# Optimization experiments

Hardware: AMD Instinct MI355X
Metric: run time of the kernel (lower is better)

Reference implementation:

```python
import jax, jax.numpy as jnp
import numpy as np

N_NODES = 10000
N_EDGES = 320000
D_IN = 256
D_OUT = 256
MAX_NORM = 0.95

def setup_inputs() -> dict:
    key = jax.random.key(0)
    ks = jax.random.split(key, 7)
    x = jax.random.normal(ks[0], (N_NODES, D_IN), dtype=jnp.float32)
    edge_index = jax.random.randint(ks[1], (2, N_EDGES), 0, N_NODES, dtype=jnp.int64)
    # xavier-ish scales
    W = jax.random.normal(ks[2], (D_OUT, D_IN), dtype=jnp.float32) * (1.0 / np.sqrt(D_IN))
    b = jax.random.normal(ks[3], (D_OUT,), dtype=jnp.float32) * 0.02
    mag_w = jax.random.normal(ks[4], (1, D_IN), dtype=jnp.float32) * 0.02
    mag_b = jax.random.normal(ks[5], (1,), dtype=jnp.float32) * 0.02
    attn_w = jax.random.normal(ks[6], (1, 2 * D_OUT), dtype=jnp.float32) * (1.0 / np.sqrt(2 * D_OUT))
    return {"x": x, "edge_index": edge_index, "W": W, "b": b,
            "mag_w": mag_w, "mag_b": mag_b, "attn_w": attn_w}

def _expmap0(u):
    # Poincare ball exp map at origin, curvature c = 1.0
    un = jnp.linalg.norm(u, axis=-1, keepdims=True)
    un_c = jnp.maximum(un, 1e-15)
    return jnp.tanh(un_c) * u / un_c

def reference(x, edge_index, W, b, mag_w, mag_b, attn_w):
    N = x.shape[0]
    F_out = W.shape[0]
    # linear transform + directional/magnitude decomposition
    h_raw = x @ W.T + b                                              # (N, F)
    h_dir = h_raw / jnp.maximum(jnp.linalg.norm(h_raw, axis=-1, keepdims=True), 1e-12)
    h_mag = jax.nn.sigmoid(x @ mag_w.T + mag_b) * 1.5                # (N, 1)
    h = h_dir * h_mag                                                # (N, F)
    src, tgt = edge_index[0], edge_index[1]
    h_src = h[src]                                                   # (E, F)
    h_tgt = h[tgt]                                                   # (E, F)
    # attn(cat([h_src, h_tgt])) == h_src @ a_s + h_tgt @ a_t (avoids concat)
    a_s, a_t = attn_w[0, :F_out], attn_w[0, F_out:]
    scores = h_src @ a_s + h_tgt @ a_t                               # (E,)
    # scatter softmax over edges grouped by target node
    mx = jnp.maximum(jax.ops.segment_max(scores, tgt, num_segments=N), -1e9)
    ex = jnp.exp(scores - mx[tgt])
    se = jax.ops.segment_sum(ex, tgt, num_segments=N)
    attn_weights = ex / (se[tgt] + 1e-10)                            # (E,)
    # weighted message aggregation
    agg = jax.ops.segment_sum(h_src * attn_weights[:, None], tgt, num_segments=N)
    h_combined = h + agg
    h_poincare = _expmap0(h_combined)
    norms = jnp.linalg.norm(h_poincare, axis=1, keepdims=True)
    return jnp.where(norms > MAX_NORM, h_poincare * (MAX_NORM / (norms + 1e-8)), h_poincare)
```

## Files before the change

### kernel.cpp

```cpp
#include <hip/hip_runtime.h>
#include <math.h>

#define N_NODES 10000
#define N_EDGES 320000
#define D 256
#define CAP 128
#define BM 32
#define LDK 40

typedef __attribute__((ext_vector_type(8))) short short8;
typedef __attribute__((ext_vector_type(4))) float f32x4;

__device__ __forceinline__ ushort f2bf(float f) {
    union { float f; unsigned u; } v; v.f = f;
    unsigned r = v.u + 0x7FFFu + ((v.u >> 16) & 1u);
    return (ushort)(r >> 16);
}
__device__ __forceinline__ float bf2f(ushort u) {
    union { unsigned u; float f; } v; v.u = (unsigned)u << 16;
    return v.f;
}

__global__ __launch_bounds__(256) void k_prep(const float* __restrict__ W,
                                              ushort* __restrict__ Wb) {
    const int i = (blockIdx.x * 256 + threadIdx.x) * 4;
    const float4 v = *(const float4*)&W[i];
    ushort4 o;
    o.x = f2bf(v.x); o.y = f2bf(v.y); o.z = f2bf(v.z); o.w = f2bf(v.w);
    *(ushort4*)&Wb[i] = o;
}

__global__ __launch_bounds__(256) void k_gemm_fused(const float* __restrict__ x,
                                                    const ushort* __restrict__ Wb,
                                                    const float* __restrict__ b,
                                                    const float* __restrict__ mag_w,
                                                    const float* __restrict__ mag_b,
                                                    const float* __restrict__ attn_w,
                                                    ushort* __restrict__ hb,
                                                    float* __restrict__ s_s,
                                                    float* __restrict__ s_t,
                                                    unsigned* __restrict__ deg) {
    __shared__ ushort ldsA[BM * LDK];
    __shared__ ushort ldsB[256 * LDK];
    __shared__ float red_ssq[4][BM], red_ra[4][BM], red_rt[4][BM];
    __shared__ float smrow[BM], scl[BM];

    const int t = threadIdx.x;
    const int w = t >> 6, l = t & 63;
    const int bm = blockIdx.x * BM;
    const int sra = t >> 3, ka = (t & 7) * 4;
    const int am = bm + sra;
    const int srb = t >> 2, kb = (t & 3) * 8;

    const int fl = l & 15;
    const int fh = (l >> 4) * 8;

    f32x4 acc[2][4];
#pragma unroll
    for (int r = 0; r < 2; ++r)
#pragma unroll
        for (int c = 0; c < 4; ++c) acc[r][c] = (f32x4)(0.f);

    float sm_part = 0.f;

    for (int k0 = 0; k0 < D; k0 += 32) {
        float4 xa = make_float4(0.f, 0.f, 0.f, 0.f);
        if (am < N_NODES) xa = *(const float4*)&x[(size_t)am * D + k0 + ka];
        const float4 mwv = *(const float4*)&mag_w[k0 + ka];
        sm_part += xa.x * mwv.x + xa.y * mwv.y + xa.z * mwv.z + xa.w * mwv.w;
        short8 bv[4];
#pragma unroll
        for (int p = 0; p < 4; ++p)
            bv[p] = *(const short8*)&Wb[(size_t)(p * 64 + srb) * D + k0 + kb];
        __syncthreads();
        ushort4 av;
        av.x = f2bf(xa.x); av.y = f2bf(xa.y); av.z = f2bf(xa.z); av.w = f2bf(xa.w);
        *(ushort4*)&ldsA[sra * LDK + ka] = av;
#pragma unroll
        for (int p = 0; p < 4; ++p)
            *(short8*)&ldsB[(p * 64 + srb) * LDK + kb] = bv[p];
        __syncthreads();
        short8 af[2], bfr[4];
#pragma unroll
        for (int r = 0; r < 2; ++r)
            af[r] = *(short8*)&ldsA[(r * 16 + fl) * LDK + fh];
#pragma unroll
        for (int c = 0; c < 4; ++c)
            bfr[c] = *(short8*)&ldsB[(w * 64 + c * 16 + fl) * LDK + fh];
#pragma unroll
        for (int r = 0; r < 2; ++r)
#pragma unroll
            for (int c = 0; c < 4; ++c)
                acc[r][c] = __builtin_amdgcn_mfma_f32_16x16x32_bf16(af[r], bfr[c], acc[r][c], 0, 0, 0);
    }

#pragma unroll
    for (int o = 1; o < 8; o <<= 1) sm_part += __shfl_xor(sm_part, o);
    if ((t & 7) == 0) smrow[sra] = sm_part;

    float bn[4], asn[4], atn[4];
#pragma unroll
    for (int c = 0; c < 4; ++c) {
        const int n = w * 64 + c * 16 + fl;
        bn[c]  = b[n];
        asn[c] = attn_w[n];
        atn[c] = attn_w[D + n];
    }
    const int rq = (l >> 4) * 4;

#pragma unroll
    for (int r = 0; r < 2; ++r) {
#pragma unroll
        for (int reg = 0; reg < 4; ++reg) {
            float vssq = 0.f, vra = 0.f, vrt = 0.f;
#pragma unroll
            for (int c = 0; c < 4; ++c) {
                const float v = acc[r][c][reg] + bn[c];
                vssq += v * v;
                vra  += v * asn[c];
                vrt  += v * atn[c];
            }
#pragma unroll
            for (int o = 1; o < 16; o <<= 1) {
                vssq += __shfl_xor(vssq, o);
                vra  += __shfl_xor(vra, o);
                vrt  += __shfl_xor(vrt, o);
            }
            if (fl == 0) {
                const int m = r * 16 + rq + reg;
                red_ssq[w][m] = vssq;
                red_ra[w][m]  = vra;
                red_rt[w][m]  = vrt;
            }
        }
    }
    __syncthreads();

    if (t < BM) {
        const int gm = bm + t;
        const float ssq = red_ssq[0][t] + red_ssq[1][t] + red_ssq[2][t] + red_ssq[3][t];
        const float ra  = red_ra[0][t]  + red_ra[1][t]  + red_ra[2][t]  + red_ra[3][t];
        const float rt  = red_rt[0][t]  + red_rt[1][t]  + red_rt[2][t]  + red_rt[3][t];
        const float norm = sqrtf(ssq);
        const float mag  = 1.5f / (1.f + expf(-(smrow[t] + mag_b[0])));
        const float scale = mag / fmaxf(norm, 1e-12f);
        scl[t] = scale;
        if (gm < N_NODES) {
            s_s[gm] = ra * scale;
            s_t[gm] = rt * scale;
            deg[gm] = 0u;
        }
    }
    __syncthreads();

#pragma unroll
    for (int r = 0; r < 2; ++r) {
#pragma unroll
        for (int reg = 0; reg < 4; ++reg) {
            const int ml = r * 16 + rq + reg;
            const int m = bm + ml;
            if (m < N_NODES) {
                const float scale = scl[ml];
#pragma unroll
                for (int c = 0; c < 4; ++c) {
                    const int n = w * 64 + c * 16 + fl;
                    hb[(size_t)m * D + n] = f2bf((acc[r][c][reg] + bn[c]) * scale);
                }
            }
        }
    }
}

__global__ void k_build(const int* __restrict__ ei,
                        unsigned* __restrict__ deg,
                        int* __restrict__ csr_src) {
    const int e = blockIdx.x * blockDim.x + threadIdx.x;
    if (e >= N_EDGES) return;
    int src = ei[e];
    int tgt = ei[N_EDGES + e];
    src = min(max(src, 0), N_NODES - 1);
    tgt = min(max(tgt, 0), N_NODES - 1);
    const unsigned slot = atomicAdd(&deg[tgt], 1u);
    if (slot < CAP) csr_src[(size_t)tgt * CAP + slot] = src;
}

__global__ __launch_bounds__(256) void k_agg(const ushort* __restrict__ hb,
                                             const unsigned* __restrict__ deg,
                                             const int* __restrict__ csr_src,
                                             const float* __restrict__ s_s,
                                             const float* __restrict__ s_t,
                                             float* __restrict__ out) {
    const int wv = threadIdx.x >> 6;
    const int n = blockIdx.x * 4 + wv;
    const int lane = threadIdx.x & 63;
    const int d = min((int)deg[n], CAP);
    const size_t cbase = (size_t)n * CAP;
    const float st_n = s_t[n];

    int src0 = 0, src1 = 0;
    float sc0 = -1e30f, sc1 = -1e30f;
    if (lane < d)      { src0 = csr_src[cbase + lane];      sc0 = s_s[src0] + st_n; }
    if (lane + 64 < d) { src1 = csr_src[cbase + lane + 64]; sc1 = s_s[src1] + st_n; }
    float mx = fmaxf(sc0, sc1);
#pragma unroll
    for (int o = 32; o > 0; o >>= 1) mx = fmaxf(mx, __shfl_xor(mx, o));
    mx = fmaxf(mx, -1e9f);
    float w0 = (lane < d)      ? expf(sc0 - mx) : 0.f;
    float w1 = (lane + 64 < d) ? expf(sc1 - mx) : 0.f;
    float sum = w0 + w1;
#pragma unroll
    for (int o = 32; o > 0; o >>= 1) sum += __shfl_xor(sum, o);
    const float inv = 1.f / (sum + 1e-10f);

    const int coff = lane * 4;
    float4 A0 = make_float4(0.f, 0.f, 0.f, 0.f), A1 = A0, A2 = A0, A3 = A0;

    {
        const int cnt = min(d, 64);
        int e = 0;
        for (; e + 4 <= cnt; e += 4) {
            const int s0 = __shfl(src0, e), s1 = __shfl(src0, e + 1);
            const int s2 = __shfl(src0, e + 2), s3 = __shfl(src0, e + 3);
            const float q0 = __shfl(w0, e) * inv,     q1 = __shfl(w0, e + 1) * inv;
            const float q2 = __shfl(w0, e + 2) * inv, q3 = __shfl(w0, e + 3) * inv;
            const ushort4 v0 = *(const ushort4*)&hb[(size_t)s0 * D + coff];
            const ushort4 v1 = *(const ushort4*)&hb[(size_t)s1 * D + coff];
            const ushort4 v2 = *(const ushort4*)&hb[(size_t)s2 * D + coff];
            const ushort4 v3 = *(const ushort4*)&hb[(size_t)s3 * D + coff];
            A0.x += q0 * bf2f(v0.x); A0.y += q0 * bf2f(v0.y); A0.z += q0 * bf2f(v0.z); A0.w += q0 * bf2f(v0.w);
            A1.x += q1 * bf2f(v1.x); A1.y += q1 * bf2f(v1.y); A1.z += q1 * bf2f(v1.z); A1.w += q1 * bf2f(v1.w);
            A2.x += q2 * bf2f(v2.x); A2.y += q2 * bf2f(v2.y); A2.z += q2 * bf2f(v2.z); A2.w += q2 * bf2f(v2.w);
            A3.x += q3 * bf2f(v3.x); A3.y += q3 * bf2f(v3.y); A3.z += q3 * bf2f(v3.z); A3.w += q3 * bf2f(v3.w);
        }
        for (; e < cnt; ++e) {
            const int s0 = __shfl(src0, e);
            const float q0 = __shfl(w0, e) * inv;
            const ushort4 v0 = *(const ushort4*)&hb[(size_t)s0 * D + coff];
            A0.x += q0 * bf2f(v0.x); A0.y += q0 * bf2f(v0.y); A0.z += q0 * bf2f(v0.z); A0.w += q0 * bf2f(v0.w);
        }
    }
    {
        const int cnt = d - 64;
        int e = 0;
        for (; e + 4 <= cnt; e += 4) {
            const int s0 = __shfl(src1, e), s1 = __shfl(src1, e + 1);
            const int s2 = __shfl(src1, e + 2), s3 = __shfl(src1, e + 3);
            const float q0 = __shfl(w1, e) * inv,     q1 = __shfl(w1, e + 1) * inv;
            const float q2 = __shfl(w1, e + 2) * inv, q3 = __shfl(w1, e + 3) * inv;
            const ushort4 v0 = *(const ushort4*)&hb[(size_t)s0 * D + coff];
            const ushort4 v1 = *(const ushort4*)&hb[(size_t)s1 * D + coff];
            const ushort4 v2 = *(const ushort4*)&hb[(size_t)s2 * D + coff];
            const ushort4 v3 = *(const ushort4*)&hb[(size_t)s3 * D + coff];
            A0.x += q0 * bf2f(v0.x); A0.y += q0 * bf2f(v0.y); A0.z += q0 * bf2f(v0.z); A0.w += q0 * bf2f(v0.w);
            A1.x += q1 * bf2f(v1.x); A1.y += q1 * bf2f(v1.y); A1.z += q1 * bf2f(v1.z); A1.w += q1 * bf2f(v1.w);
            A2.x += q2 * bf2f(v2.x); A2.y += q2 * bf2f(v2.y); A2.z += q2 * bf2f(v2.z); A2.w += q2 * bf2f(v2.w);
            A3.x += q3 * bf2f(v3.x); A3.y += q3 * bf2f(v3.y); A3.z += q3 * bf2f(v3.z); A3.w += q3 * bf2f(v3.w);
        }
        for (; e < cnt; ++e) {
            const int s0 = __shfl(src1, e);
            const float q0 = __shfl(w1, e) * inv;
            const ushort4 v0 = *(const ushort4*)&hb[(size_t)s0 * D + coff];
            A0.x += q0 * bf2f(v0.x); A0.y += q0 * bf2f(v0.y); A0.z += q0 * bf2f(v0.z); A0.w += q0 * bf2f(v0.w);
        }
    }
    float4 acc = make_float4(A0.x + A1.x + A2.x + A3.x,
                             A0.y + A1.y + A2.y + A3.y,
                             A0.z + A1.z + A2.z + A3.z,
                             A0.w + A1.w + A2.w + A3.w);

    const ushort4 hnv = *(const ushort4*)&hb[(size_t)n * D + coff];
    float4 u = make_float4(bf2f(hnv.x) + acc.x, bf2f(hnv.y) + acc.y,
                           bf2f(hnv.z) + acc.z, bf2f(hnv.w) + acc.w);
    float ssq = u.x * u.x + u.y * u.y + u.z * u.z + u.w * u.w;
#pragma unroll
    for (int o = 32; o > 0; o >>= 1) ssq += __shfl_xor(ssq, o);
    const float un = sqrtf(ssq);
    const float un_c = fmaxf(un, 1e-15f);
    const float th = tanhf(un_c);
    float s = th / un_c;
    const float pn = th * (un / un_c);
    if (pn > 0.95f) s *= 0.95f / (pn + 1e-8f);
    float4 p = make_float4(u.x * s, u.y * s, u.z * s, u.w * s);
    *(float4*)&out[(size_t)n * D + coff] = p;
}

extern "C" void kernel_launch(void* const* d_in, const int* in_sizes, int n_in,
                              void* d_out, int out_size, void* d_ws, size_t ws_size,
                              hipStream_t stream) {
    const float* x      = (const float*)d_in[0];
    const int*   ei     = (const int*)d_in[1];
    const float* W      = (const float*)d_in[2];
    const float* b      = (const float*)d_in[3];
    const float* mag_w  = (const float*)d_in[4];
    const float* mag_b  = (const float*)d_in[5];
    const float* attn_w = (const float*)d_in[6];
    float* out = (float*)d_out;

    char* ws = (char*)d_ws;
    ushort* hb = (ushort*)ws;         ws += (size_t)N_NODES * D * sizeof(ushort);
    float* s_s = (float*)ws;          ws += (size_t)N_NODES * sizeof(float);
    float* s_t = (float*)ws;          ws += (size_t)N_NODES * sizeof(float);
    unsigned* deg = (unsigned*)ws;    ws += (size_t)N_NODES * sizeof(unsigned);
    int* csr_src = (int*)ws;          ws += (size_t)N_NODES * CAP * sizeof(int);
    ushort* Wb = (ushort*)ws;         ws += (size_t)D * D * sizeof(ushort);

    k_prep<<<(D * D) / (256 * 4), 256, 0, stream>>>(W, Wb);
    k_gemm_fused<<<(N_NODES + BM - 1) / BM, 256, 0, stream>>>(
        x, Wb, b, mag_w, mag_b, attn_w, hb, s_s, s_t, deg);
    k_build<<<(N_EDGES + 255) / 256, 256, 0, stream>>>(ei, deg, csr_src);
    k_agg<<<N_NODES / 4, 256, 0, stream>>>(hb, deg, csr_src, s_s, s_t, out);
}
```

Baseline: 68.41 us.

## Cancel target score in softmax and merge CSR build into GEMM launch

The per-target score term is constant within each softmax group, so it cancels. The GEMM now stores exp(source score) per node, and the aggregation kernel drops the max reduction, the exp calls and the target-score loads. Normalization by the sum is applied once after accumulation instead of on every edge weight. The CSR build blocks are appended to the GEMM grid so both run in one launch and can overlap, and the degree reset moves into the weight-prep kernel. Dropping max subtraction assumes the scores stay small enough that exp cannot overflow, which holds only while the attention weights and node norms are bounded.

```diff
diff --git a/kernel.cpp b/kernel.cpp
--- a/kernel.cpp
+++ b/kernel.cpp
@@ -7,6 +7,8 @@
 #define CAP 128
 #define BM 32
 #define LDK 40
+#define GB_GEMM ((N_NODES + BM - 1) / BM)
+#define GB_BUILD ((N_EDGES + 255) / 256)
 
 typedef __attribute__((ext_vector_type(8))) short short8;
 typedef __attribute__((ext_vector_type(4))) float f32x4;
@@ -22,27 +24,44 @@
 }
 
 __global__ __launch_bounds__(256) void k_prep(const float* __restrict__ W,
-                                              ushort* __restrict__ Wb) {
-    const int i = (blockIdx.x * 256 + threadIdx.x) * 4;
+                                              ushort* __restrict__ Wb,
+                                              unsigned* __restrict__ deg) {
+    const int tid = blockIdx.x * 256 + threadIdx.x;
+    const int i = tid * 4;
     const float4 v = *(const float4*)&W[i];
     ushort4 o;
     o.x = f2bf(v.x); o.y = f2bf(v.y); o.z = f2bf(v.z); o.w = f2bf(v.w);
     *(ushort4*)&Wb[i] = o;
-}
-
-__global__ __launch_bounds__(256) void k_gemm_fused(const float* __restrict__ x,
-                                                    const ushort* __restrict__ Wb,
-                                                    const float* __restrict__ b,
-                                                    const float* __restrict__ mag_w,
-                                                    const float* __restrict__ mag_b,
-                                                    const float* __restrict__ attn_w,
-                                                    ushort* __restrict__ hb,
-                                                    float* __restrict__ s_s,
-                                                    float* __restrict__ s_t,
-                                                    unsigned* __restrict__ deg) {
+    if (tid < N_NODES) deg[tid] = 0u;
+}
+
+__global__ __launch_bounds__(256) void k_main(const float* __restrict__ x,
+                                              const ushort* __restrict__ Wb,
+                                              const float* __restrict__ b,
+                                              const float* __restrict__ mag_w,
+                                              const float* __restrict__ mag_b,
+                                              const float* __restrict__ attn_w,
+                                              const int* __restrict__ ei,
+                                              unsigned* __restrict__ deg,
+                                              int* __restrict__ csr_src,
+                                              ushort* __restrict__ hb,
+                                              float* __restrict__ es) {
+    if (blockIdx.x >= GB_GEMM) {
+        const int e = (blockIdx.x - GB_GEMM) * 256 + threadIdx.x;
+        if (e < N_EDGES) {
+            int src = ei[e];
+            int tgt = ei[N_EDGES + e];
+            src = min(max(src, 0), N_NODES - 1);
+            tgt = min(max(tgt, 0), N_NODES - 1);
+            const unsigned slot = atomicAdd(&deg[tgt], 1u);
+            if (slot < CAP) csr_src[(size_t)tgt * CAP + slot] = src;
+        }
+        return;
+    }
+
     __shared__ ushort ldsA[BM * LDK];
     __shared__ ushort ldsB[256 * LDK];
-    __shared__ float red_ssq[4][BM], red_ra[4][BM], red_rt[4][BM];
+    __shared__ float red_ssq[4][BM], red_ra[4][BM];
     __shared__ float smrow[BM], scl[BM];
 
     const int t = threadIdx.x;
@@ -98,13 +117,12 @@
     for (int o = 1; o < 8; o <<= 1) sm_part += __shfl_xor(sm_part, o);
     if ((t & 7) == 0) smrow[sra] = sm_part;
 
-    float bn[4], asn[4], atn[4];
+    float bn[4], asn[4];
 #pragma unroll
     for (int c = 0; c < 4; ++c) {
         const int n = w * 64 + c * 16 + fl;
         bn[c]  = b[n];
         asn[c] = attn_w[n];
-        atn[c] = attn_w[D + n];
     }
     const int rq = (l >> 4) * 4;
 
@@ -112,25 +130,22 @@
     for (int r = 0; r < 2; ++r) {
 #pragma unroll
         for (int reg = 0; reg < 4; ++reg) {
-            float vssq = 0.f, vra = 0.f, vrt = 0.f;
+            float vssq = 0.f, vra = 0.f;
 #pragma unroll
             for (int c = 0; c < 4; ++c) {
                 const float v = acc[r][c][reg] + bn[c];
                 vssq += v * v;
                 vra  += v * asn[c];
-                vrt  += v * atn[c];
             }
 #pragma unroll
             for (int o = 1; o < 16; o <<= 1) {
                 vssq += __shfl_xor(vssq, o);
                 vra  += __shfl_xor(vra, o);
-                vrt  += __shfl_xor(vrt, o);
             }
             if (fl == 0) {
                 const int m = r * 16 + rq + reg;
                 red_ssq[w][m] = vssq;
                 red_ra[w][m]  = vra;
-                red_rt[w][m]  = vrt;
             }
         }
     }
@@ -140,16 +155,11 @@
         const int gm = bm + t;
         const float ssq = red_ssq[0][t] + red_ssq[1][t] + red_ssq[2][t] + red_ssq[3][t];
         const float ra  = red_ra[0][t]  + red_ra[1][t]  + red_ra[2][t]  + red_ra[3][t];
-        const float rt  = red_rt[0][t]  + red_rt[1][t]  + red_rt[2][t]  + red_rt[3][t];
         const float norm = sqrtf(ssq);
         const float mag  = 1.5f / (1.f + expf(-(smrow[t] + mag_b[0])));
         const float scale = mag / fmaxf(norm, 1e-12f);
         scl[t] = scale;
-        if (gm < N_NODES) {
-            s_s[gm] = ra * scale;
-            s_t[gm] = rt * scale;
-            deg[gm] = 0u;
-        }
+        if (gm < N_NODES) es[gm] = expf(ra * scale);
     }
     __syncthreads();
 
@@ -171,42 +181,21 @@
     }
 }
 
-__global__ void k_build(const int* __restrict__ ei,
-                        unsigned* __restrict__ deg,
-                        int* __restrict__ csr_src) {
-    const int e = blockIdx.x * blockDim.x + threadIdx.x;
-    if (e >= N_EDGES) return;
-    int src = ei[e];
-    int tgt = ei[N_EDGES + e];
-    src = min(max(src, 0), N_NODES - 1);
-    tgt = min(max(tgt, 0), N_NODES - 1);
-    const unsigned slot = atomicAdd(&deg[tgt], 1u);
-    if (slot < CAP) csr_src[(size_t)tgt * CAP + slot] = src;
-}
-
 __global__ __launch_bounds__(256) void k_agg(const ushort* __restrict__ hb,
                                              const unsigned* __restrict__ deg,
                                              const int* __restrict__ csr_src,
-                                             const float* __restrict__ s_s,
-                                             const float* __restrict__ s_t,
+                                             const float* __restrict__ es,
                                              float* __restrict__ out) {
     const int wv = threadIdx.x >> 6;
     const int n = blockIdx.x * 4 + wv;
     const int lane = threadIdx.x & 63;
     const int d = min((int)deg[n], CAP);
     const size_t cbase = (size_t)n * CAP;
-    const float st_n = s_t[n];
 
     int src0 = 0, src1 = 0;
-    float sc0 = -1e30f, sc1 = -1e30f;
-    if (lane < d)      { src0 = csr_src[cbase + lane];      sc0 = s_s[src0] + st_n; }
-    if (lane + 64 < d) { src1 = csr_src[cbase + lane + 64]; sc1 = s_s[src1] + st_n; }
-    float mx = fmaxf(sc0, sc1);
-#pragma unroll
-    for (int o = 32; o > 0; o >>= 1) mx = fmaxf(mx, __shfl_xor(mx, o));
-    mx = fmaxf(mx, -1e9f);
-    float w0 = (lane < d)      ? expf(sc0 - mx) : 0.f;
-    float w1 = (lane + 64 < d) ? expf(sc1 - mx) : 0.f;
+    float w0 = 0.f, w1 = 0.f;
+    if (lane < d)      { src0 = csr_src[cbase + lane];      w0 = es[src0]; }
+    if (lane + 64 < d) { src1 = csr_src[cbase + lane + 64]; w1 = es[src1]; }
     float sum = w0 + w1;
 #pragma unroll
     for (int o = 32; o > 0; o >>= 1) sum += __shfl_xor(sum, o);
@@ -221,8 +210,8 @@
         for (; e + 4 <= cnt; e += 4) {
             const int s0 = __shfl(src0, e), s1 = __shfl(src0, e + 1);
             const int s2 = __shfl(src0, e + 2), s3 = __shfl(src0, e + 3);
-            const float q0 = __shfl(w0, e) * inv,     q1 = __shfl(w0, e + 1) * inv;
-            const float q2 = __shfl(w0, e + 2) * inv, q3 = __shfl(w0, e + 3) * inv;
+            const float q0 = __shfl(w0, e),     q1 = __shfl(w0, e + 1);
+            const float q2 = __shfl(w0, e + 2), q3 = __shfl(w0, e + 3);
             const ushort4 v0 = *(const ushort4*)&hb[(size_t)s0 * D + coff];
             const ushort4 v1 = *(const ushort4*)&hb[(size_t)s1 * D + coff];
             const ushort4 v2 = *(const ushort4*)&hb[(size_t)s2 * D + coff];
@@ -234,19 +223,19 @@
         }
         for (; e < cnt; ++e) {
             const int s0 = __shfl(src0, e);
-            const float q0 = __shfl(w0, e) * inv;
-            const ushort4 v0 = *(const ushort4*)&hb[(size_t)s0 * D + coff];
-            A0.x += q0 * bf2f(v0.x); A0.y += q0 * bf2f(v0.y); A0.z += q0 * bf2f(v0.z); A0.w += q0 * bf2f(v0.w);
-        }
-    }
-    {
+            const float q0 = __shfl(w0, e);
+            const ushort4 v0 = *(const ushort4*)&hb[(size_t)s0 * D + coff];
+            A0.x += q0 * bf2f(v0.x); A0.y += q0 * bf2f(v0.y); A0.z += q0 * bf2f(v0.z); A0.w += q0 * bf2f(v0.w);
+        }
+    }
+    if (d > 64) {
         const int cnt = d - 64;
         int e = 0;
         for (; e + 4 <= cnt; e += 4) {
             const int s0 = __shfl(src1, e), s1 = __shfl(src1, e + 1);
             const int s2 = __shfl(src1, e + 2), s3 = __shfl(src1, e + 3);
-            const float q0 = __shfl(w1, e) * inv,     q1 = __shfl(w1, e + 1) * inv;
-            const float q2 = __shfl(w1, e + 2) * inv, q3 = __shfl(w1, e + 3) * inv;
+            const float q0 = __shfl(w1, e),     q1 = __shfl(w1, e + 1);
+            const float q2 = __shfl(w1, e + 2), q3 = __shfl(w1, e + 3);
             const ushort4 v0 = *(const ushort4*)&hb[(size_t)s0 * D + coff];
             const ushort4 v1 = *(const ushort4*)&hb[(size_t)s1 * D + coff];
             const ushort4 v2 = *(const ushort4*)&hb[(size_t)s2 * D + coff];
@@ -258,15 +247,15 @@
         }
         for (; e < cnt; ++e) {
             const int s0 = __shfl(src1, e);
-            const float q0 = __shfl(w1, e) * inv;
-            const ushort4 v0 = *(const ushort4*)&hb[(size_t)s0 * D + coff];
-            A0.x += q0 * bf2f(v0.x); A0.y += q0 * bf2f(v0.y); A0.z += q0 * bf2f(v0.z); A0.w += q0 * bf2f(v0.w);
-        }
-    }
-    float4 acc = make_float4(A0.x + A1.x + A2.x + A3.x,
-                             A0.y + A1.y + A2.y + A3.y,
-                             A0.z + A1.z + A2.z + A3.z,
-                             A0.w + A1.w + A2.w + A3.w);
+            const float q0 = __shfl(w1, e);
+            const ushort4 v0 = *(const ushort4*)&hb[(size_t)s0 * D + coff];
+            A0.x += q0 * bf2f(v0.x); A0.y += q0 * bf2f(v0.y); A0.z += q0 * bf2f(v0.z); A0.w += q0 * bf2f(v0.w);
+        }
+    }
+    float4 acc = make_float4((A0.x + A1.x + A2.x + A3.x) * inv,
+                             (A0.y + A1.y + A2.y + A3.y) * inv,
+                             (A0.z + A1.z + A2.z + A3.z) * inv,
+                             (A0.w + A1.w + A2.w + A3.w) * inv);
 
     const ushort4 hnv = *(const ushort4*)&hb[(size_t)n * D + coff];
     float4 u = make_float4(bf2f(hnv.x) + acc.x, bf2f(hnv.y) + acc.y,
@@ -298,15 +287,13 @@
 
     char* ws = (char*)d_ws;
     ushort* hb = (ushort*)ws;         ws += (size_t)N_NODES * D * sizeof(ushort);
-    float* s_s = (float*)ws;          ws += (size_t)N_NODES * sizeof(float);
-    float* s_t = (float*)ws;          ws += (size_t)N_NODES * sizeof(float);
+    float* es = (float*)ws;           ws += (size_t)N_NODES * sizeof(float);
     unsigned* deg = (unsigned*)ws;    ws += (size_t)N_NODES * sizeof(unsigned);
     int* csr_src = (int*)ws;          ws += (size_t)N_NODES * CAP * sizeof(int);
     ushort* Wb = (ushort*)ws;         ws += (size_t)D * D * sizeof(ushort);
 
-    k_prep<<<(D * D) / (256 * 4), 256, 0, stream>>>(W, Wb);
-    k_gemm_fused<<<(N_NODES + BM - 1) / BM, 256, 0, stream>>>(
-        x, Wb, b, mag_w, mag_b, attn_w, hb, s_s, s_t, deg);
-    k_build<<<(N_EDGES + 255) / 256, 256, 0, stream>>>(ei, deg, csr_src);
-    k_agg<<<N_NODES / 4, 256, 0, stream>>>(hb, deg, csr_src, s_s, s_t, out);
-}
+    k_prep<<<(D * D) / (256 * 4), 256, 0, stream>>>(W, Wb, deg);
+    k_main<<<GB_GEMM + GB_BUILD, 256, 0, stream>>>(
+        x, Wb, b, mag_w, mag_b, attn_w, ei, deg, csr_src, hb, es);
+    k_agg<<<N_NODES / 4, 256, 0, stream>>>(hb, deg, csr_src, es, out);
+}
```

After: 57.83 us. 15.5% less time.
